# Performance work log

Measured on AMD Instinct MI355X. Metric: run time of the kernel, lower is better.

## Reference

```python
import jax, jax.numpy as jnp
import numpy as np

B, N, Q, H = 32, 1024, 64, 768


def setup_inputs() -> dict:
    key = jax.random.key(0)
    k1, k2, k3, k4 = jax.random.split(key, 4)
    return {
        "nodes_compress": jax.random.normal(k1, (B, N, H), dtype=jnp.float32),
        "query_compress": jax.random.normal(k2, (B, Q, H), dtype=jnp.float32),
        "nodes_hidden": jax.random.normal(k3, (B, N, H), dtype=jnp.float32),
        # nn.Linear(3H, 1, bias=False).weight flattened to (3H,)
        "w": jax.random.normal(k4, (3 * H,), dtype=jnp.float32) * (1.0 / np.sqrt(3 * H)),
    }


def reference(nodes_compress, query_compress, nodes_hidden, w):
    h = nodes_compress.shape[-1]
    w_n, w_q, w_nq = w[:h], w[h:2 * h], w[2 * h:]
    # Decomposed trilinear similarity: identical to Linear([n, q, n*q]) -> scalar
    sim = (
        (nodes_compress @ w_n)[:, :, None]          # (B, N, 1)
        + (query_compress @ w_q)[:, None, :]        # (B, 1, Q)
        + jnp.einsum("bnh,bqh,h->bnq", nodes_compress, query_compress, w_nq)
    )                                                # (B, N, Q)
    # nodes -> query attention
    a = jax.nn.softmax(sim, axis=-1)                 # (B, N, Q)
    nodes2query = jnp.einsum("bnq,bqh->bnh", a, query_compress)
    # query -> nodes attention (max over query, softmax over nodes)
    b = jax.nn.softmax(jnp.max(sim, axis=-1), axis=-1)  # (B, N)
    q2n = jnp.einsum("bn,bnh->bh", b, nodes_compress)[:, None, :]  # (B, 1, H)
    q2n = jnp.broadcast_to(q2n, nodes_compress.shape)               # (B, N, H)
    return jnp.concatenate(
        [nodes_compress, nodes2query, nodes_compress * nodes2query, nodes_compress * q2n],
        axis=-1,
    )  # (B, N, 4H)
```

## Files before the change

### kernel.cpp

```cpp
#include <hip/hip_runtime.h>
#include <hip/hip_bf16.h>

#define BB 32
#define NN 1024
#define QQ 64
#define HH 768

typedef __attribute__((ext_vector_type(8))) short short8;
typedef __attribute__((ext_vector_type(4))) float f32x4;

#define GLOAD_LDS16(gp, lp) \
  __builtin_amdgcn_global_load_lds((const __attribute__((address_space(1))) unsigned int*)(gp), \
                                   (__attribute__((address_space(3))) unsigned int*)(lp), 16, 0, 0)

__device__ __forceinline__ unsigned short f2b(float f) {
  unsigned int u = __float_as_uint(f);
  unsigned int r = u + 0x7fffu + ((u >> 16) & 1u);
  return (unsigned short)(r >> 16);
}

__device__ __forceinline__ unsigned int pk2(float a, float b) {
  __hip_bfloat162 t = __float22bfloat162_rn(make_float2(a, b));
  union { __hip_bfloat162 h; unsigned int u; } c;
  c.h = t;
  return c.u;
}

__device__ __forceinline__ short8 cvt8(float4 f0, float4 f1) {
  union { short8 s; unsigned int u[4]; } o;
  o.u[0] = pk2(f0.x, f0.y);
  o.u[1] = pk2(f0.z, f0.w);
  o.u[2] = pk2(f1.x, f1.y);
  o.u[3] = pk2(f1.z, f1.w);
  return o.s;
}

__global__ __launch_bounds__(256) void k_prep(
    const float* __restrict__ qc, const float* __restrict__ w,
    unsigned short* __restrict__ qwB, unsigned short* __restrict__ qcT,
    float* __restrict__ sq_part) {
  __shared__ float qcL[128][66];

  const int tid = threadIdx.x;
  const int bid = blockIdx.x;
  const int b = bid / 6, hc = bid % 6;
  const float* qcB = qc + (size_t)(b * 64) * HH + hc * 128;

#pragma unroll
  for (int i = 0; i < 8; ++i) {
    int u = i * 256 + tid;
    int q = u >> 5, c4 = u & 31;
    float4 v = *(const float4*)(qcB + (size_t)q * HH + c4 * 4);
    qcL[c4 * 4 + 0][q] = v.x;
    qcL[c4 * 4 + 1][q] = v.y;
    qcL[c4 * 4 + 2][q] = v.z;
    qcL[c4 * 4 + 3][q] = v.w;
  }
  __syncthreads();

  {
    char* dst = (char*)qwB + ((size_t)bid << 14);
#pragma unroll
    for (int i = 0; i < 4; ++i) {
      int p = i * 256 + tid;
      int q = p >> 4, uu = p & 15;
      int hg = hc * 128 + uu * 8;
      float e[8];
#pragma unroll
      for (int j = 0; j < 8; ++j)
        e[j] = qcL[uu * 8 + j][q] * w[2 * HH + hg + j] + w[hg + j];
      union { short8 s; unsigned int u4[4]; } o;
      o.u4[0] = pk2(e[0], e[1]); o.u4[1] = pk2(e[2], e[3]);
      o.u4[2] = pk2(e[4], e[5]); o.u4[3] = pk2(e[6], e[7]);
      *(short8*)(dst + ((size_t)(q * 16 + (uu ^ (q & 7)))) * 16) = o.s;
    }
  }
  {
    char* dst = (char*)qcT + ((size_t)bid << 14);
#pragma unroll
    for (int i = 0; i < 4; ++i) {
      int p = i * 256 + tid;
      int r = p >> 3, x = p & 7;
      int xu = x ^ (r & 7);
      union { short8 s; unsigned int u4[4]; } o;
#pragma unroll
      for (int j = 0; j < 4; ++j)
        o.u4[j] = pk2(qcL[r][xu * 8 + j * 2], qcL[r][xu * 8 + j * 2 + 1]);
      *(short8*)(dst + (size_t)p * 16) = o.s;
    }
  }
  {
    int q = tid >> 2, qt = tid & 3;
    float s = 0.f;
#pragma unroll
    for (int k = 0; k < 32; ++k)
      s += qcL[qt * 32 + k][q] * w[HH + hc * 128 + qt * 32 + k];
    s += __shfl_xor(s, 1);
    s += __shfl_xor(s, 2);
    if (qt == 0) sq_part[bid * 64 + q] = s;
  }
}

__global__ __launch_bounds__(256) void k_sim(
    const float* __restrict__ nc, const unsigned short* __restrict__ qwB,
    const float* __restrict__ sq_part, float* __restrict__ partial,
    float* __restrict__ mtse, unsigned short* __restrict__ probs)
{
  __shared__ __align__(16) char bbuf[3][16384];
  __shared__ float rowmF[64];
  __shared__ float wvF[64];
  __shared__ float pW[4][768];

  const int tid = threadIdx.x;
  const int wv_ = tid >> 6, l = tid & 63;
  const int l15 = l & 15, lg = l >> 4;
  const int lb = (blockIdx.x & 7) * 64 + (blockIdx.x >> 3);
  const int b = lb >> 4, tile = lb & 15;
  const int row0 = tile * 64;

  const float* ncB = nc + (size_t)(b * NN + row0) * HH;
  const char* qwb = (const char*)qwB + (size_t)b * 98304;
  const float* aBase = ncB + (wv_ * 16 + l15) * HH + lg * 8;

  {
    const char* gsrc = qwb + wv_ * 4096 + l * 16;
#pragma unroll
    for (int i = 0; i < 4; ++i)
      GLOAD_LDS16(gsrc + i * 1024, &bbuf[0][wv_ * 4096 + i * 1024]);
  }
  float4 fr[2][8];
#pragma unroll
  for (int ks = 0; ks < 4; ++ks) {
    fr[0][ks * 2]     = *(const float4*)(aBase + ks * 32);
    fr[0][ks * 2 + 1] = *(const float4*)(aBase + ks * 32 + 4);
  }

  f32x4 acc[4] = {};
#pragma unroll
  for (int kc = 0; kc < 6; ++kc) {
    short8 af[4];
#pragma unroll
    for (int ks = 0; ks < 4; ++ks)
      af[ks] = cvt8(fr[kc & 1][ks * 2], fr[kc & 1][ks * 2 + 1]);
    if (kc < 5) {
#pragma unroll
      for (int ks = 0; ks < 4; ++ks) {
        fr[(kc + 1) & 1][ks * 2]     = *(const float4*)(aBase + (kc + 1) * 128 + ks * 32);
        fr[(kc + 1) & 1][ks * 2 + 1] = *(const float4*)(aBase + (kc + 1) * 128 + ks * 32 + 4);
      }
      const char* gsrc = qwb + (kc + 1) * 16384 + wv_ * 4096 + l * 16;
#pragma unroll
      for (int i = 0; i < 4; ++i)
        GLOAD_LDS16(gsrc + i * 1024, &bbuf[(kc + 1) % 3][wv_ * 4096 + i * 1024]);
      asm volatile("s_waitcnt vmcnt(12)" ::: "memory");
    } else {
      asm volatile("s_waitcnt vmcnt(0)" ::: "memory");
    }
    __builtin_amdgcn_s_barrier();
    __builtin_amdgcn_sched_barrier(0);
#pragma unroll
    for (int ks = 0; ks < 4; ++ks) {
      int kbyte = ks * 64 + lg * 16;
#pragma unroll
      for (int nt = 0; nt < 4; ++nt) {
        int brow = nt * 16 + l15;
        short8 bf = *(short8*)(&bbuf[kc % 3][0] + brow * 256 + (kbyte ^ ((l & 7) << 4)));
        acc[nt] = __builtin_amdgcn_mfma_f32_16x16x32_bf16(af[ks], bf, acc[nt], 0, 0, 0);
      }
    }
    __builtin_amdgcn_sched_barrier(0);
  }
  __syncthreads();

  unsigned short* pT = probs + (size_t)(b * 16 + tile) * (QQ * QQ);
  float sqv[4];
#pragma unroll
  for (int nt = 0; nt < 4; ++nt) {
    float s = 0.f;
#pragma unroll
    for (int i = 0; i < 6; ++i) s += sq_part[(b * 6 + i) * 64 + nt * 16 + l15];
    sqv[nt] = s;
  }
#pragma unroll
  for (int j = 0; j < 4; ++j) {
    float mm = -1e30f;
#pragma unroll
    for (int nt = 0; nt < 4; ++nt) { acc[nt][j] += sqv[nt]; mm = fmaxf(mm, acc[nt][j]); }
    mm = fmaxf(mm, __shfl_xor(mm, 1));
    mm = fmaxf(mm, __shfl_xor(mm, 2));
    mm = fmaxf(mm, __shfl_xor(mm, 4));
    mm = fmaxf(mm, __shfl_xor(mm, 8));
    float ss = 0.f;
#pragma unroll
    for (int nt = 0; nt < 4; ++nt) { float p = __expf(acc[nt][j] - mm); acc[nt][j] = p; ss += p; }
    ss += __shfl_xor(ss, 1); ss += __shfl_xor(ss, 2);
    ss += __shfl_xor(ss, 4); ss += __shfl_xor(ss, 8);
    float inv = 1.0f / ss;
    int r = wv_ * 16 + lg * 4 + j;
#pragma unroll
    for (int nt = 0; nt < 4; ++nt)
      pT[r * 64 + nt * 16 + l15] = f2b(acc[nt][j] * inv);
    if (l15 == 0) rowmF[r] = mm;
  }
  __syncthreads();

  float m_t = -1e30f;
#pragma unroll
  for (int i = 0; i < 16; ++i) {
    f32x4 v = ((f32x4*)rowmF)[i];
    m_t = fmaxf(m_t, fmaxf(fmaxf(v[0], v[1]), fmaxf(v[2], v[3])));
  }
  if (tid < 64) wvF[tid] = __expf(rowmF[tid] - m_t);
  __syncthreads();
  {
    float sv = wvF[l];
#pragma unroll
    for (int m = 1; m < 64; m <<= 1) sv += __shfl_xor(sv, m);
    if (tid == 0) {
      mtse[(b * 16 + tile) * 2] = m_t;
      mtse[(b * 16 + tile) * 2 + 1] = sv;
    }
  }
  {
    f32x4 a3[3] = {};
    for (int n0 = 0; n0 < 16; ++n0) {
      int n = wv_ * 16 + n0;
      float wvv = wvF[n];
      const float* pr = ncB + (size_t)n * HH;
#pragma unroll
      for (int j = 0; j < 3; ++j) {
        f32x4 v = *(const f32x4*)(pr + j * 256 + l * 4);
        a3[j] += v * wvv;
      }
    }
#pragma unroll
    for (int j = 0; j < 3; ++j)
      *(f32x4*)(&pW[wv_][j * 256 + l * 4]) = a3[j];
  }
  __syncthreads();
  {
    float* pp = partial + (size_t)(b * 16 + tile) * HH + tid;
    pp[0]   = pW[0][tid]       + pW[1][tid]       + pW[2][tid]       + pW[3][tid];
    pp[256] = pW[0][tid + 256] + pW[1][tid + 256] + pW[2][tid + 256] + pW[3][tid + 256];
    pp[512] = pW[0][tid + 512] + pW[1][tid + 512] + pW[2][tid + 512] + pW[3][tid + 512];
  }
}

__global__ __launch_bounds__(256) void k_out(
    const float* __restrict__ nc, const unsigned short* __restrict__ qcT,
    const unsigned short* __restrict__ probs, const float* __restrict__ partial,
    const float* __restrict__ mtse, float* __restrict__ out)
{
  __shared__ __align__(16) char smem[16384];
  __shared__ float q2nL[128];

  const int tid = threadIdx.x;
  const int wv_ = tid >> 6, l = tid & 63;
  const int l15 = l & 15, lg = l >> 4;
  const int lb = (blockIdx.x & 7) * 384 + (blockIdx.x >> 3);
  const int hc = lb % 6;
  const int bt = lb / 6;
  const int b = bt >> 4, tile = bt & 15;
  const int row0 = tile * 64;

  {
    const char* src = (const char*)qcT + ((size_t)(b * 6 + hc) << 14) + wv_ * 4096 + l * 16;
#pragma unroll
    for (int i = 0; i < 4; ++i)
      GLOAD_LDS16(src + i * 1024, &smem[wv_ * 4096 + i * 1024]);
  }

  if (tid < 128) {
    float M = -1e30f, mt[16], se[16];
#pragma unroll
    for (int i = 0; i < 16; ++i) {
      mt[i] = mtse[(b * 16 + i) * 2];
      se[i] = mtse[(b * 16 + i) * 2 + 1];
      M = fmaxf(M, mt[i]);
    }
    float denom = 0.f;
#pragma unroll
    for (int i = 0; i < 16; ++i) { mt[i] = __expf(mt[i] - M); denom += mt[i] * se[i]; }
    float inv = 1.0f / denom;
    float a = 0.f;
#pragma unroll
    for (int i = 0; i < 16; ++i)
      a += mt[i] * partial[(size_t)(b * 16 + i) * HH + hc * 128 + tid];
    q2nL[tid] = a * inv;
  }

  const unsigned short* pT = probs + (size_t)bt * (QQ * QQ);
  short8 a2_0 = *(const short8*)((const char*)pT + (wv_ * 16 + l15) * 128 + lg * 16);
  short8 a2_1 = *(const short8*)((const char*)pT + (wv_ * 16 + l15) * 128 + 64 + lg * 16);

  asm volatile("s_waitcnt vmcnt(0)" ::: "memory");
  __syncthreads();

  const int n = wv_ * 16 + l15;
  const float* ncrow = nc + (size_t)(b * NN + row0 + n) * HH;
  float* orow = out + (size_t)(b * NN + row0 + n) * 3072;

#pragma unroll
  for (int hg = 0; hg < 8; ++hg) {
    f32x4 c2 = {};
#pragma unroll
    for (int ks2 = 0; ks2 < 2; ++ks2) {
      int hrow = hg * 16 + l15;
      int kbyte = ks2 * 64 + lg * 16;
      short8 hf = *(short8*)(&smem[0] + hrow * 128 + (kbyte ^ ((l & 7) << 4)));
      c2 = __builtin_amdgcn_mfma_f32_16x16x32_bf16(hf, ks2 ? a2_1 : a2_0, c2, 0, 0, 0);
    }
    int hl = hg * 16 + lg * 4;
    int hbase = hc * 128 + hl;
    f32x4 ncv = *(const f32x4*)(ncrow + hbase);
    f32x4 qv  = *(const f32x4*)(&q2nL[hl]);
    *(f32x4*)(orow + hbase)          = ncv;
    *(f32x4*)(orow + HH + hbase)     = c2;
    *(f32x4*)(orow + 2 * HH + hbase) = ncv * c2;
    *(f32x4*)(orow + 2304 + hbase)   = ncv * qv;
  }
}

extern "C" void kernel_launch(void* const* d_in, const int* in_sizes, int n_in,
                              void* d_out, int out_size, void* d_ws, size_t ws_size,
                              hipStream_t stream) {
  (void)in_sizes; (void)n_in; (void)out_size; (void)ws_size;
  const float* nc = (const float*)d_in[0];
  const float* qc = (const float*)d_in[1];
  const float* w  = (const float*)d_in[3];
  float* out = (float*)d_out;
  char* ws = (char*)d_ws;
  unsigned short* qwB = (unsigned short*)(ws);
  unsigned short* qcT = (unsigned short*)(ws + 3145728);
  float* sq_part = (float*)(ws + 6291456);
  float* partial = (float*)(ws + 6340608);
  float* mtse    = (float*)(ws + 7913472);
  unsigned short* probs = (unsigned short*)(ws + 7917568);

  k_prep<<<192, 256, 0, stream>>>(qc, w, qwB, qcT, sq_part);
  k_sim<<<512, 256, 0, stream>>>(nc, qwB, sq_part, partial, mtse, probs);
  k_out<<<3072, 256, 0, stream>>>(nc, qcT, probs, partial, mtse, out);
}
```

Before: 156.1 us.

## Split sim kernel over query halves and move softmax stats to new kernel

```diff
diff --git a/kernel.cpp b/kernel.cpp
--- a/kernel.cpp
+++ b/kernel.cpp
@@ -103,30 +103,29 @@
 
 __global__ __launch_bounds__(256) void k_sim(
     const float* __restrict__ nc, const unsigned short* __restrict__ qwB,
-    const float* __restrict__ sq_part, float* __restrict__ partial,
-    float* __restrict__ mtse, unsigned short* __restrict__ probs)
+    const float* __restrict__ sq_part, unsigned short* __restrict__ probs,
+    float* __restrict__ mh)
 {
-  __shared__ __align__(16) char bbuf[3][16384];
-  __shared__ float rowmF[64];
-  __shared__ float wvF[64];
-  __shared__ float pW[4][768];
+  __shared__ __align__(16) char bbuf[3][8192];
 
   const int tid = threadIdx.x;
   const int wv_ = tid >> 6, l = tid & 63;
   const int l15 = l & 15, lg = l >> 4;
-  const int lb = (blockIdx.x & 7) * 64 + (blockIdx.x >> 3);
-  const int b = lb >> 4, tile = lb & 15;
+  const int lb = (blockIdx.x & 7) * 128 + (blockIdx.x >> 3);
+  const int b = lb >> 5, rem = lb & 31;
+  const int tile = rem >> 1, qh = rem & 1;
+  const int bt = b * 16 + tile;
   const int row0 = tile * 64;
 
   const float* ncB = nc + (size_t)(b * NN + row0) * HH;
-  const char* qwb = (const char*)qwB + (size_t)b * 98304;
+  const char* qwb = (const char*)qwB + (size_t)b * 98304 + qh * 8192;
   const float* aBase = ncB + (wv_ * 16 + l15) * HH + lg * 8;
 
   {
-    const char* gsrc = qwb + wv_ * 4096 + l * 16;
-#pragma unroll
-    for (int i = 0; i < 4; ++i)
-      GLOAD_LDS16(gsrc + i * 1024, &bbuf[0][wv_ * 4096 + i * 1024]);
+    const char* gsrc = qwb + wv_ * 2048 + l * 16;
+#pragma unroll
+    for (int i = 0; i < 2; ++i)
+      GLOAD_LDS16(gsrc + i * 1024, &bbuf[0][wv_ * 2048 + i * 1024]);
   }
   float4 fr[2][8];
 #pragma unroll
@@ -135,7 +134,7 @@
     fr[0][ks * 2 + 1] = *(const float4*)(aBase + ks * 32 + 4);
   }
 
-  f32x4 acc[4] = {};
+  f32x4 acc[2] = {};
 #pragma unroll
   for (int kc = 0; kc < 6; ++kc) {
     short8 af[4];
@@ -148,11 +147,11 @@
         fr[(kc + 1) & 1][ks * 2]     = *(const float4*)(aBase + (kc + 1) * 128 + ks * 32);
         fr[(kc + 1) & 1][ks * 2 + 1] = *(const float4*)(aBase + (kc + 1) * 128 + ks * 32 + 4);
       }
-      const char* gsrc = qwb + (kc + 1) * 16384 + wv_ * 4096 + l * 16;
-#pragma unroll
-      for (int i = 0; i < 4; ++i)
-        GLOAD_LDS16(gsrc + i * 1024, &bbuf[(kc + 1) % 3][wv_ * 4096 + i * 1024]);
-      asm volatile("s_waitcnt vmcnt(12)" ::: "memory");
+      const char* gsrc = qwb + (kc + 1) * 16384 + wv_ * 2048 + l * 16;
+#pragma unroll
+      for (int i = 0; i < 2; ++i)
+        GLOAD_LDS16(gsrc + i * 1024, &bbuf[(kc + 1) % 3][wv_ * 2048 + i * 1024]);
+      asm volatile("s_waitcnt vmcnt(10)" ::: "memory");
     } else {
       asm volatile("s_waitcnt vmcnt(0)" ::: "memory");
     }
@@ -162,7 +161,7 @@
     for (int ks = 0; ks < 4; ++ks) {
       int kbyte = ks * 64 + lg * 16;
 #pragma unroll
-      for (int nt = 0; nt < 4; ++nt) {
+      for (int nt = 0; nt < 2; ++nt) {
         int brow = nt * 16 + l15;
         short8 bf = *(short8*)(&bbuf[kc % 3][0] + brow * 256 + (kbyte ^ ((l & 7) << 4)));
         acc[nt] = __builtin_amdgcn_mfma_f32_16x16x32_bf16(af[ks], bf, acc[nt], 0, 0, 0);
@@ -170,37 +169,68 @@
     }
     __builtin_amdgcn_sched_barrier(0);
   }
-  __syncthreads();
-
-  unsigned short* pT = probs + (size_t)(b * 16 + tile) * (QQ * QQ);
-  float sqv[4];
-#pragma unroll
-  for (int nt = 0; nt < 4; ++nt) {
+
+  unsigned short* pT = probs + (size_t)bt * (QQ * QQ);
+  float sqv[2];
+#pragma unroll
+  for (int nt = 0; nt < 2; ++nt) {
     float s = 0.f;
 #pragma unroll
-    for (int i = 0; i < 6; ++i) s += sq_part[(b * 6 + i) * 64 + nt * 16 + l15];
+    for (int i = 0; i < 6; ++i)
+      s += sq_part[(b * 6 + i) * 64 + qh * 32 + nt * 16 + l15];
     sqv[nt] = s;
   }
 #pragma unroll
   for (int j = 0; j < 4; ++j) {
     float mm = -1e30f;
 #pragma unroll
-    for (int nt = 0; nt < 4; ++nt) { acc[nt][j] += sqv[nt]; mm = fmaxf(mm, acc[nt][j]); }
+    for (int nt = 0; nt < 2; ++nt) { acc[nt][j] += sqv[nt]; mm = fmaxf(mm, acc[nt][j]); }
     mm = fmaxf(mm, __shfl_xor(mm, 1));
     mm = fmaxf(mm, __shfl_xor(mm, 2));
     mm = fmaxf(mm, __shfl_xor(mm, 4));
     mm = fmaxf(mm, __shfl_xor(mm, 8));
     float ss = 0.f;
 #pragma unroll
-    for (int nt = 0; nt < 4; ++nt) { float p = __expf(acc[nt][j] - mm); acc[nt][j] = p; ss += p; }
+    for (int nt = 0; nt < 2; ++nt) { float p = __expf(acc[nt][j] - mm); acc[nt][j] = p; ss += p; }
     ss += __shfl_xor(ss, 1); ss += __shfl_xor(ss, 2);
     ss += __shfl_xor(ss, 4); ss += __shfl_xor(ss, 8);
-    float inv = 1.0f / ss;
     int r = wv_ * 16 + lg * 4 + j;
 #pragma unroll
-    for (int nt = 0; nt < 4; ++nt)
-      pT[r * 64 + nt * 16 + l15] = f2b(acc[nt][j] * inv);
-    if (l15 == 0) rowmF[r] = mm;
+    for (int nt = 0; nt < 2; ++nt)
+      pT[r * 64 + qh * 32 + nt * 16 + l15] = f2b(acc[nt][j]);
+    if (l15 == 0) {
+      mh[((size_t)bt * 64 + r) * 4 + qh * 2]     = mm;
+      mh[((size_t)bt * 64 + r) * 4 + qh * 2 + 1] = ss;
+    }
+  }
+}
+
+__global__ __launch_bounds__(256) void k_stats(
+    const float* __restrict__ nc, const float* __restrict__ mh,
+    float* __restrict__ alphas, float* __restrict__ mtse,
+    float* __restrict__ partial)
+{
+  __shared__ float rowmF[64];
+  __shared__ float wvF[64];
+  __shared__ float pW[4][768];
+
+  const int tid = threadIdx.x;
+  const int wv_ = tid >> 6, l = tid & 63;
+  const int lb = (blockIdx.x & 7) * 64 + (blockIdx.x >> 3);
+  const int b = lb >> 4, tile = lb & 15;
+  const int bt = b * 16 + tile;
+  const int row0 = tile * 64;
+  const float* ncB = nc + (size_t)(b * NN + row0) * HH;
+
+  if (tid < 64) {
+    const float* m4 = mh + ((size_t)bt * 64 + tid) * 4;
+    float m0 = m4[0], s0 = m4[1], m1 = m4[2], s1 = m4[3];
+    float M = fmaxf(m0, m1);
+    float a0 = __expf(m0 - M), a1 = __expf(m1 - M);
+    float inv = 1.0f / (a0 * s0 + a1 * s1);
+    alphas[((size_t)bt * 64 + tid) * 2]     = a0 * inv;
+    alphas[((size_t)bt * 64 + tid) * 2 + 1] = a1 * inv;
+    rowmF[tid] = M;
   }
   __syncthreads();
 
@@ -217,8 +247,8 @@
 #pragma unroll
     for (int m = 1; m < 64; m <<= 1) sv += __shfl_xor(sv, m);
     if (tid == 0) {
-      mtse[(b * 16 + tile) * 2] = m_t;
-      mtse[(b * 16 + tile) * 2 + 1] = sv;
+      mtse[bt * 2] = m_t;
+      mtse[bt * 2 + 1] = sv;
     }
   }
   {
@@ -239,7 +269,7 @@
   }
   __syncthreads();
   {
-    float* pp = partial + (size_t)(b * 16 + tile) * HH + tid;
+    float* pp = partial + (size_t)bt * HH + tid;
     pp[0]   = pW[0][tid]       + pW[1][tid]       + pW[2][tid]       + pW[3][tid];
     pp[256] = pW[0][tid + 256] + pW[1][tid + 256] + pW[2][tid + 256] + pW[3][tid + 256];
     pp[512] = pW[0][tid + 512] + pW[1][tid + 512] + pW[2][tid + 512] + pW[3][tid + 512];
@@ -249,7 +279,8 @@
 __global__ __launch_bounds__(256) void k_out(
     const float* __restrict__ nc, const unsigned short* __restrict__ qcT,
     const unsigned short* __restrict__ probs, const float* __restrict__ partial,
-    const float* __restrict__ mtse, float* __restrict__ out)
+    const float* __restrict__ mtse, const float* __restrict__ alphas,
+    float* __restrict__ out)
 {
   __shared__ __align__(16) char smem[16384];
   __shared__ float q2nL[128];
@@ -289,27 +320,29 @@
     q2nL[tid] = a * inv;
   }
 
+  const int n = wv_ * 16 + l15;
   const unsigned short* pT = probs + (size_t)bt * (QQ * QQ);
-  short8 a2_0 = *(const short8*)((const char*)pT + (wv_ * 16 + l15) * 128 + lg * 16);
-  short8 a2_1 = *(const short8*)((const char*)pT + (wv_ * 16 + l15) * 128 + 64 + lg * 16);
+  short8 a2_0 = *(const short8*)((const char*)pT + n * 128 + lg * 16);
+  short8 a2_1 = *(const short8*)((const char*)pT + n * 128 + 64 + lg * 16);
+  float2 al = *(const float2*)(alphas + ((size_t)bt * 64 + n) * 2);
 
   asm volatile("s_waitcnt vmcnt(0)" ::: "memory");
   __syncthreads();
 
-  const int n = wv_ * 16 + l15;
   const float* ncrow = nc + (size_t)(b * NN + row0 + n) * HH;
   float* orow = out + (size_t)(b * NN + row0 + n) * 3072;
 
 #pragma unroll
   for (int hg = 0; hg < 8; ++hg) {
-    f32x4 c2 = {};
-#pragma unroll
-    for (int ks2 = 0; ks2 < 2; ++ks2) {
+    f32x4 c2h0 = {}, c2h1 = {};
+    {
       int hrow = hg * 16 + l15;
-      int kbyte = ks2 * 64 + lg * 16;
-      short8 hf = *(short8*)(&smem[0] + hrow * 128 + (kbyte ^ ((l & 7) << 4)));
-      c2 = __builtin_amdgcn_mfma_f32_16x16x32_bf16(hf, ks2 ? a2_1 : a2_0, c2, 0, 0, 0);
-    }
+      short8 hf0 = *(short8*)(&smem[0] + hrow * 128 + ((lg * 16) ^ ((l & 7) << 4)));
+      c2h0 = __builtin_amdgcn_mfma_f32_16x16x32_bf16(hf0, a2_0, c2h0, 0, 0, 0);
+      short8 hf1 = *(short8*)(&smem[0] + hrow * 128 + ((64 + lg * 16) ^ ((l & 7) << 4)));
+      c2h1 = __builtin_amdgcn_mfma_f32_16x16x32_bf16(hf1, a2_1, c2h1, 0, 0, 0);
+    }
+    f32x4 c2 = c2h0 * al.x + c2h1 * al.y;
     int hl = hg * 16 + lg * 4;
     int hbase = hc * 128 + hl;
     f32x4 ncv = *(const f32x4*)(ncrow + hbase);
@@ -336,8 +369,11 @@
   float* partial = (float*)(ws + 6340608);
   float* mtse    = (float*)(ws + 7913472);
   unsigned short* probs = (unsigned short*)(ws + 7917568);
+  float* mh      = (float*)(ws + 12111872);
+  float* alphas  = (float*)(ws + 12636160);
 
   k_prep<<<192, 256, 0, stream>>>(qc, w, qwB, qcT, sq_part);
-  k_sim<<<512, 256, 0, stream>>>(nc, qwB, sq_part, partial, mtse, probs);
-  k_out<<<3072, 256, 0, stream>>>(nc, qcT, probs, partial, mtse, out);
-}
+  k_sim<<<1024, 256, 0, stream>>>(nc, qwB, sq_part, probs, mh);
+  k_stats<<<512, 256, 0, stream>>>(nc, mh, alphas, mtse, partial);
+  k_out<<<3072, 256, 0, stream>>>(nc, qcT, probs, partial, mtse, alphas, out);
+}
```

Measured after the change: 179.0 us. +14.7%, slower.

## Split k_sim columns across two wave groups using 512-thread blocks

Applied to the files above, without the earlier changes.

```diff
diff --git a/kernel.cpp b/kernel.cpp
--- a/kernel.cpp
+++ b/kernel.cpp
@@ -101,32 +101,34 @@
   }
 }
 
-__global__ __launch_bounds__(256) void k_sim(
+__global__ __launch_bounds__(512, 4) void k_sim(
     const float* __restrict__ nc, const unsigned short* __restrict__ qwB,
     const float* __restrict__ sq_part, float* __restrict__ partial,
     float* __restrict__ mtse, unsigned short* __restrict__ probs)
 {
   __shared__ __align__(16) char bbuf[3][16384];
+  __shared__ float redM[2][64];
+  __shared__ float redS[2][64];
   __shared__ float rowmF[64];
   __shared__ float wvF[64];
-  __shared__ float pW[4][768];
+  __shared__ float pW[8][768];
 
   const int tid = threadIdx.x;
   const int wv_ = tid >> 6, l = tid & 63;
   const int l15 = l & 15, lg = l >> 4;
+  const int rw = wv_ & 3, cw = wv_ >> 2;
   const int lb = (blockIdx.x & 7) * 64 + (blockIdx.x >> 3);
   const int b = lb >> 4, tile = lb & 15;
   const int row0 = tile * 64;
 
   const float* ncB = nc + (size_t)(b * NN + row0) * HH;
   const char* qwb = (const char*)qwB + (size_t)b * 98304;
-  const float* aBase = ncB + (wv_ * 16 + l15) * HH + lg * 8;
-
-  {
-    const char* gsrc = qwb + wv_ * 4096 + l * 16;
-#pragma unroll
-    for (int i = 0; i < 4; ++i)
-      GLOAD_LDS16(gsrc + i * 1024, &bbuf[0][wv_ * 4096 + i * 1024]);
+  const float* aBase = ncB + (rw * 16 + l15) * HH + lg * 8;
+
+  {
+    const char* gsrc = qwb + tid * 16;
+    GLOAD_LDS16(gsrc, &bbuf[0][tid * 16]);
+    GLOAD_LDS16(gsrc + 8192, &bbuf[0][tid * 16 + 8192]);
   }
   float4 fr[2][8];
 #pragma unroll
@@ -135,7 +137,7 @@
     fr[0][ks * 2 + 1] = *(const float4*)(aBase + ks * 32 + 4);
   }
 
-  f32x4 acc[4] = {};
+  f32x4 acc[2] = {};
 #pragma unroll
   for (int kc = 0; kc < 6; ++kc) {
     short8 af[4];
@@ -148,11 +150,10 @@
         fr[(kc + 1) & 1][ks * 2]     = *(const float4*)(aBase + (kc + 1) * 128 + ks * 32);
         fr[(kc + 1) & 1][ks * 2 + 1] = *(const float4*)(aBase + (kc + 1) * 128 + ks * 32 + 4);
       }
-      const char* gsrc = qwb + (kc + 1) * 16384 + wv_ * 4096 + l * 16;
-#pragma unroll
-      for (int i = 0; i < 4; ++i)
-        GLOAD_LDS16(gsrc + i * 1024, &bbuf[(kc + 1) % 3][wv_ * 4096 + i * 1024]);
-      asm volatile("s_waitcnt vmcnt(12)" ::: "memory");
+      const char* gsrc = qwb + (kc + 1) * 16384 + tid * 16;
+      GLOAD_LDS16(gsrc, &bbuf[(kc + 1) % 3][tid * 16]);
+      GLOAD_LDS16(gsrc + 8192, &bbuf[(kc + 1) % 3][tid * 16 + 8192]);
+      asm volatile("s_waitcnt vmcnt(10)" ::: "memory");
     } else {
       asm volatile("s_waitcnt vmcnt(0)" ::: "memory");
     }
@@ -162,8 +163,8 @@
     for (int ks = 0; ks < 4; ++ks) {
       int kbyte = ks * 64 + lg * 16;
 #pragma unroll
-      for (int nt = 0; nt < 4; ++nt) {
-        int brow = nt * 16 + l15;
+      for (int nt = 0; nt < 2; ++nt) {
+        int brow = (cw * 2 + nt) * 16 + l15;
         short8 bf = *(short8*)(&bbuf[kc % 3][0] + brow * 256 + (kbyte ^ ((l & 7) << 4)));
         acc[nt] = __builtin_amdgcn_mfma_f32_16x16x32_bf16(af[ks], bf, acc[nt], 0, 0, 0);
       }
@@ -173,36 +174,50 @@
   __syncthreads();
 
   unsigned short* pT = probs + (size_t)(b * 16 + tile) * (QQ * QQ);
-  float sqv[4];
-#pragma unroll
-  for (int nt = 0; nt < 4; ++nt) {
+  float sqv[2];
+#pragma unroll
+  for (int nt = 0; nt < 2; ++nt) {
     float s = 0.f;
 #pragma unroll
-    for (int i = 0; i < 6; ++i) s += sq_part[(b * 6 + i) * 64 + nt * 16 + l15];
+    for (int i = 0; i < 6; ++i)
+      s += sq_part[(b * 6 + i) * 64 + cw * 32 + nt * 16 + l15];
     sqv[nt] = s;
   }
 #pragma unroll
   for (int j = 0; j < 4; ++j) {
     float mm = -1e30f;
 #pragma unroll
-    for (int nt = 0; nt < 4; ++nt) { acc[nt][j] += sqv[nt]; mm = fmaxf(mm, acc[nt][j]); }
+    for (int nt = 0; nt < 2; ++nt) { acc[nt][j] += sqv[nt]; mm = fmaxf(mm, acc[nt][j]); }
     mm = fmaxf(mm, __shfl_xor(mm, 1));
     mm = fmaxf(mm, __shfl_xor(mm, 2));
     mm = fmaxf(mm, __shfl_xor(mm, 4));
     mm = fmaxf(mm, __shfl_xor(mm, 8));
+    if (l15 == 0) redM[cw][rw * 16 + lg * 4 + j] = mm;
+  }
+  __syncthreads();
+#pragma unroll
+  for (int j = 0; j < 4; ++j) {
+    int r = rw * 16 + lg * 4 + j;
+    float mm = fmaxf(redM[0][r], redM[1][r]);
     float ss = 0.f;
 #pragma unroll
-    for (int nt = 0; nt < 4; ++nt) { float p = __expf(acc[nt][j] - mm); acc[nt][j] = p; ss += p; }
+    for (int nt = 0; nt < 2; ++nt) { float p = __expf(acc[nt][j] - mm); acc[nt][j] = p; ss += p; }
     ss += __shfl_xor(ss, 1); ss += __shfl_xor(ss, 2);
     ss += __shfl_xor(ss, 4); ss += __shfl_xor(ss, 8);
-    float inv = 1.0f / ss;
-    int r = wv_ * 16 + lg * 4 + j;
-#pragma unroll
-    for (int nt = 0; nt < 4; ++nt)
-      pT[r * 64 + nt * 16 + l15] = f2b(acc[nt][j] * inv);
-    if (l15 == 0) rowmF[r] = mm;
-  }
-  __syncthreads();
+    if (l15 == 0) {
+      redS[cw][r] = ss;
+      if (cw == 0) rowmF[r] = mm;
+    }
+  }
+  __syncthreads();
+#pragma unroll
+  for (int j = 0; j < 4; ++j) {
+    int r = rw * 16 + lg * 4 + j;
+    float inv = 1.0f / (redS[0][r] + redS[1][r]);
+#pragma unroll
+    for (int nt = 0; nt < 2; ++nt)
+      pT[r * 64 + cw * 32 + nt * 16 + l15] = f2b(acc[nt][j] * inv);
+  }
 
   float m_t = -1e30f;
 #pragma unroll
@@ -223,8 +238,8 @@
   }
   {
     f32x4 a3[3] = {};
-    for (int n0 = 0; n0 < 16; ++n0) {
-      int n = wv_ * 16 + n0;
+    for (int n0 = 0; n0 < 8; ++n0) {
+      int n = wv_ * 8 + n0;
       float wvv = wvF[n];
       const float* pr = ncB + (size_t)n * HH;
 #pragma unroll
@@ -238,11 +253,15 @@
       *(f32x4*)(&pW[wv_][j * 256 + l * 4]) = a3[j];
   }
   __syncthreads();
-  {
+  if (tid < 256) {
     float* pp = partial + (size_t)(b * 16 + tile) * HH + tid;
-    pp[0]   = pW[0][tid]       + pW[1][tid]       + pW[2][tid]       + pW[3][tid];
-    pp[256] = pW[0][tid + 256] + pW[1][tid + 256] + pW[2][tid + 256] + pW[3][tid + 256];
-    pp[512] = pW[0][tid + 512] + pW[1][tid + 512] + pW[2][tid + 512] + pW[3][tid + 512];
+#pragma unroll
+    for (int c = 0; c < 3; ++c) {
+      float s = 0.f;
+#pragma unroll
+      for (int wgi = 0; wgi < 8; ++wgi) s += pW[wgi][tid + c * 256];
+      pp[c * 256] = s;
+    }
   }
 }
 
@@ -338,6 +357,6 @@
   unsigned short* probs = (unsigned short*)(ws + 7917568);
 
   k_prep<<<192, 256, 0, stream>>>(qc, w, qwB, qcT, sq_part);
-  k_sim<<<512, 256, 0, stream>>>(nc, qwB, sq_part, partial, mtse, probs);
+  k_sim<<<512, 512, 0, stream>>>(nc, qwB, sq_part, partial, mtse, probs);
   k_out<<<3072, 256, 0, stream>>>(nc, qcT, probs, partial, mtse, out);
 }
```

Measured after the change: 169.8 us. 1.09x slower.
